# Optimization experiments

Hardware: AMD Instinct MI355X
Metric: run time of the kernel (lower is better)

The kernel has to match this reference:

```python
import jax, jax.numpy as jnp
import numpy as np


def _relative_index(ih: int, iw: int) -> np.ndarray:
    # Static precompute mirroring the torch buffer.
    yy, xx = np.meshgrid(np.arange(ih), np.arange(iw), indexing='ij')
    coords = np.stack([yy.ravel(), xx.ravel()])                 # [2, n]
    rel = coords[:, :, None] - coords[:, None, :]               # [2, n, n]
    rel[0] += ih - 1
    rel[1] += iw - 1
    rel[0] *= 2 * iw - 1
    return rel.sum(0).ravel()                                   # [n*n]


def setup_inputs() -> dict:
    key = jax.random.key(0)
    ks = jax.random.split(key, 5)
    B, N, INP, OUP, HEADS = 64, 256, 512, 512, 16
    ih = iw = 16
    return {
        'x': jax.random.normal(ks[0], (B, N, INP), jnp.float32),
        'w_qkv': jax.random.normal(ks[1], (INP, 3 * OUP), jnp.float32) * 0.02,
        'rel_bias_table': jax.random.normal(ks[2], ((2 * ih - 1) * (2 * iw - 1), HEADS), jnp.float32) * 0.02,
        'w_out': jax.random.normal(ks[3], (OUP, OUP), jnp.float32) * 0.02,
        'b_out': jax.random.normal(ks[4], (OUP,), jnp.float32) * 0.02,
        'ih': ih,
        'iw': iw,
    }


def reference(x, w_qkv, rel_bias_table, w_out, b_out, ih, iw):
    B, N, _ = x.shape
    heads = rel_bias_table.shape[1]
    oup = w_out.shape[0]
    dim_head = oup // heads
    scale = dim_head ** -0.5

    qkv = jnp.einsum('bni,ij->bnj', x, w_qkv)                   # [B, N, 3*oup]
    q, k, v = jnp.split(qkv, 3, axis=-1)
    split_heads = lambda t: t.reshape(B, N, heads, dim_head).transpose(0, 2, 1, 3)
    q, k, v = split_heads(q), split_heads(k), split_heads(v)    # [B, H, N, D]

    dots = jnp.einsum('bhnd,bhmd->bhnm', q, k) * scale          # [B, H, N, N]
    rel_idx = jnp.asarray(_relative_index(int(ih), int(iw)))    # [N*N]
    bias = rel_bias_table[rel_idx].reshape(N, N, heads)         # gather
    dots = dots + bias.transpose(2, 0, 1)[None]                 # [1, H, N, N]

    attn = jax.nn.softmax(dots, axis=-1)
    out = jnp.einsum('bhnm,bhmd->bhnd', attn, v)                # [B, H, N, D]
    out = out.transpose(0, 2, 1, 3).reshape(B, N, oup)
    return jnp.einsum('bno,op->bnp', out, w_out.T) + b_out
```

## Files before the change

### kernel.cpp

```cpp
#include <hip/hip_runtime.h>
#include <stdint.h>

typedef unsigned short u16;
typedef unsigned int u32;
typedef __attribute__((ext_vector_type(8))) __bf16 bf16x8;
typedef __attribute__((ext_vector_type(2))) u32 u32x2;
typedef __attribute__((ext_vector_type(4))) u32 u32x4;
typedef __attribute__((ext_vector_type(4))) float f32x4;

__device__ __forceinline__ float bf2f(u16 x) { return __uint_as_float(((u32)x) << 16); }
__device__ __forceinline__ u16 f2bf(float f) {
  u32 u = __float_as_uint(f);
  u32 r = (u + 0x7fffu + ((u >> 16) & 1u)) >> 16;
  return (u16)r;
}
__device__ __forceinline__ u16 cvbf(float f) {
  union { __bf16 b; u16 u; } x;
  x.b = (__bf16)f;
  return x.u;
}

__device__ __forceinline__ u32x2 ld8(const u16* p) { return *(const u32x2*)p; }
__device__ __forceinline__ u32x4 ld16(const u16* p) { return *(const u32x4*)p; }
__device__ __forceinline__ bf16x8 mk_frag(u32x2 lo, u32x2 hi) {
  union { bf16x8 v; u32x2 u[2]; } t;
  t.u[0] = lo; t.u[1] = hi;
  return t.v;
}

__device__ __forceinline__ void stage_fm(u16* lds, int ch, u32x4 v) {
  int row = ch >> 2, q = ch & 3;
  *(u32x4*)&lds[(row >> 4) * 512 + q * 128 + (row & 15) * 8] = v;
}

__device__ __forceinline__ bf16x8 frag_fm(const u16* lds, int subtile, int g, int c) {
  union { bf16x8 v; u32x4 u; } t;
  t.u = ld16(&lds[subtile * 512 + g * 128 + c * 8]);
  return t.v;
}

__device__ __forceinline__ void swz_bn_bm(int& bn, int& bm) {
  const u32 nx = gridDim.x, ny = gridDim.y;
  if ((ny & 7u) == 0u) {
    u32 d = blockIdx.y * nx + blockIdx.x;
    u32 xcd = d & 7u, wi = d >> 3;
    bm = (int)(xcd * (ny >> 3) + wi / nx);
    bn = (int)(wi % nx);
  } else {
    bn = blockIdx.x;
    bm = blockIdx.y;
  }
}

__global__ void probe_dtype(const u32* __restrict__ x, u32* __restrict__ flag) {
  if (threadIdx.x == 0 && blockIdx.x == 0) {
    int cnt = 0;
    for (int i = 0; i < 32; ++i) {
      u32 e = (x[i] >> 7) & 0xffu;
      cnt += (e >= 96u && e <= 140u) ? 1 : 0;
    }
    *flag = (cnt == 32) ? 1u : 0u;
  }
}

__global__ __launch_bounds__(256) void conv4(const void* __restrict__ src, u16* __restrict__ dst,
                                             const u32* __restrict__ flag, int n4) {
  const bool isbf = (*flag != 0u);
  const int stride = gridDim.x * 256;
  for (int i = blockIdx.x * 256 + threadIdx.x; i < n4; i += stride) {
    if (isbf) {
      ((u32x2*)dst)[i] = ((const u32x2*)src)[i];
    } else {
      const float* s = (const float*)src + (size_t)i * 4;
      u32x2 o;
      o.x = (u32)f2bf(s[0]) | ((u32)f2bf(s[1]) << 16);
      o.y = (u32)f2bf(s[2]) | ((u32)f2bf(s[3]) << 16);
      ((u32x2*)dst)[i] = o;
    }
  }
}

__global__ __launch_bounds__(256) void bias_prep(const void* __restrict__ table,
                                                 float* __restrict__ biasT,
                                                 const u32* __restrict__ flag) {
  const bool isbf = (*flag != 0u);
  int i = blockIdx.x * 256 + threadIdx.x;
  if (i < 16 * 961) {
    int h = i / 961, idx = i - h * 961;
    float v = isbf ? bf2f(((const u16*)table)[idx * 16 + h])
                   : ((const float*)table)[idx * 16 + h];
    biasT[i] = v * 1.4426950408889634f;
  }
}

__global__ __launch_bounds__(256) void transpose_dt(const void* __restrict__ in,
                                                    u16* __restrict__ out,
                                                    const u32* __restrict__ flag, int R, int C) {
  __shared__ u16 t[32][33];
  const bool isbf = (*flag != 0u);
  int r0 = blockIdx.y * 32, c0 = blockIdx.x * 32;
  int rr = threadIdx.x >> 5, cc = threadIdx.x & 31;
#pragma unroll
  for (int i = 0; i < 4; ++i) {
    size_t idx = (size_t)(r0 + rr + i * 8) * C + c0 + cc;
    t[rr + i * 8][cc] = isbf ? ((const u16*)in)[idx] : f2bf(((const float*)in)[idx]);
  }
  __syncthreads();
#pragma unroll
  for (int i = 0; i < 4; ++i) out[(size_t)(c0 + rr + i * 8) * R + r0 + cc] = t[cc][rr + i * 8];
}

template <bool BIAS>
__global__ __launch_bounds__(256) void gemm_k512(const u16* __restrict__ A,
                                                 const u16* __restrict__ BT,
                                                 const u16* __restrict__ bias,
                                                 void* __restrict__ O, int ldo, int row0g,
                                                 const u32* __restrict__ flag) {
  constexpr int K = 512;
  constexpr int NT = 16;
  __shared__ u16 As[128 * 32];
  __shared__ u16 Bs[128 * 32];
  const int tid = threadIdx.x;
  const int wave = tid >> 6, lane = tid & 63;
  const int c = lane & 15, g = lane >> 4;
  const int wm = wave >> 1, wn = wave & 1;
  int bn, bm;
  swz_bn_bm(bn, bm);

  const u16* Ab = A + (size_t)bm * 128 * K;
  const u16* Bb = BT + (size_t)bn * 128 * K;

  const int row0 = tid >> 2, q0 = tid & 3;
  const u16* Asrc0 = Ab + (size_t)row0 * K + q0 * 8;
  const u16* Bsrc0 = Bb + (size_t)row0 * K + q0 * 8;
  const u16* Asrc1 = Asrc0 + (size_t)64 * K;
  const u16* Bsrc1 = Bsrc0 + (size_t)64 * K;

  f32x4 acc[4][4] = {};

  u32x4 a0 = ld16(Asrc0), b0 = ld16(Bsrc0), a1 = ld16(Asrc1), b1 = ld16(Bsrc1);

#pragma unroll
  for (int t = 0; t < NT; ++t) {
    if (t > 0) {
      asm volatile("s_waitcnt lgkmcnt(0)" ::: "memory");
      __builtin_amdgcn_s_barrier();
      __builtin_amdgcn_sched_barrier(0);
    }
    stage_fm(As, tid, a0);
    stage_fm(Bs, tid, b0);
    stage_fm(As, tid + 256, a1);
    stage_fm(Bs, tid + 256, b1);
    if (t + 1 < NT) {
      const int k0 = (t + 1) * 32;
      a0 = ld16(Asrc0 + k0);
      b0 = ld16(Bsrc0 + k0);
      a1 = ld16(Asrc1 + k0);
      b1 = ld16(Bsrc1 + k0);
    }
    asm volatile("s_waitcnt lgkmcnt(0)" ::: "memory");
    __builtin_amdgcn_s_barrier();
    __builtin_amdgcn_sched_barrier(0);

    bf16x8 af[4], bfr[4];
#pragma unroll
    for (int i = 0; i < 4; ++i) {
      af[i] = frag_fm(As, wm * 4 + i, g, c);
      bfr[i] = frag_fm(Bs, wn * 4 + i, g, c);
    }
#pragma unroll
    for (int i = 0; i < 4; ++i)
#pragma unroll
      for (int j = 0; j < 4; ++j)
        acc[i][j] = __builtin_amdgcn_mfma_f32_16x16x32_bf16(af[i], bfr[j], acc[i][j], 0, 0, 0);
  }

  const bool isbf = BIAS ? (*flag != 0u) : true;
#pragma unroll
  for (int i = 0; i < 4; ++i)
#pragma unroll
    for (int j = 0; j < 4; ++j) {
      int jg = bn * 128 + wn * 64 + j * 16 + c;
      float bv = BIAS ? bf2f(bias[jg]) : 0.0f;
#pragma unroll
      for (int r = 0; r < 4; ++r) {
        int mg = bm * 128 + wm * 64 + i * 16 + 4 * g + r;
        float v = acc[i][j][r] + bv;
        size_t off = (size_t)(row0g + mg) * ldo + jg;
        if (BIAS) {
          if (isbf) ((u16*)O)[off] = f2bf(v);
          else ((float*)O)[off] = v;
        } else {
          ((u16*)O)[off] = f2bf(v);
        }
      }
    }
}

__global__ __launch_bounds__(256) void attn_kernel(const u16* __restrict__ qkv,
                                                   const float* __restrict__ biasT,
                                                   u16* __restrict__ Out) {
  __shared__ u16 smem[18432];
  float* biasS = (float*)&smem[16384];

  const int tid = threadIdx.x;
  const int wave = tid >> 6, lane = tid & 63;
  const int c = lane & 15, g = lane >> 4;
  const int half = blockIdx.x & 1;
  const int h = (blockIdx.x >> 1) & 15;
  const int b = blockIdx.x >> 5;

  const u16* xb = qkv + (size_t)b * 256 * 1536;

  u32x4 kvr[4];
#pragma unroll
  for (int i = 0; i < 4; ++i) {
    int ch = tid + i * 256;
    int m = ch >> 2;
    kvr[i] = ld16(xb + (size_t)m * 1536 + 512 + h * 32 + (ch & 3) * 8);
  }
#pragma unroll
  for (int i = 0; i < 4; ++i) stage_fm(smem, tid + i * 256, kvr[i]);

#pragma unroll
  for (int i = 0; i < 16; ++i) {
    int e2 = tid + i * 256;
    int n = e2 >> 4, d = (e2 & 15) * 2;
    u32 val = *(const u32*)(xb + (size_t)n * 1536 + 1024 + h * 32 + d);
    smem[8192 + d * 256 + (n ^ (8 * (d & 7)))] = (u16)(val & 0xffffu);
    smem[8192 + (d + 1) * 256 + (n ^ (8 * ((d + 1) & 7)))] = (u16)(val >> 16);
  }
  for (int i = tid; i < 961; i += 256) biasS[i] = biasT[h * 961 + i];

  u32x4 qv[2];
#pragma unroll
  for (int rg = 0; rg < 2; ++rg) {
    const u16* qp = xb + (size_t)((half * 2 + rg) * 64 + wave * 16 + c) * 1536 + h * 32 + 8 * g;
    qv[rg] = ld16(qp);
  }
  __syncthreads();

  const u16* Vt = &smem[8192];
  const int va = 8 * (c & 7);
  const float scale2 = 0.25503484f;
  const float* bp0 = biasS + wave * 31 + c + 12 - 4 * g;

#pragma unroll
  for (int rg = 0; rg < 2; ++rg) {
    const int rgg = half * 2 + rg;
    union { bf16x8 v; u32x4 u; } qt;
    qt.u = qv[rg];
    bf16x8 qf = qt.v;

    f32x4 o0 = {0.f, 0.f, 0.f, 0.f}, o1 = {0.f, 0.f, 0.f, 0.f};
    float smm = 0.f;

#pragma unroll
    for (int ph = 0; ph < 2; ++ph) {
      f32x4 s[8];
#pragma unroll
      for (int f = 0; f < 8; ++f) {
        bf16x8 kf = frag_fm(smem, ph * 8 + f, g, c);
        f32x4 z = {0.f, 0.f, 0.f, 0.f};
        s[f] = __builtin_amdgcn_mfma_f32_16x16x32_bf16(kf, qf, z, 0, 0, 0);
      }

      float u[8];
#pragma unroll
      for (int f = 0; f < 8; ++f) {
        const int fg = ph * 8 + f;
#pragma unroll
        for (int j = 0; j < 4; ++j) {
          float bv = bp0[(rgg * 4 - fg + 15) * 31 + 3 - j];
          s[f][j] = __builtin_amdgcn_exp2f(s[f][j] * scale2 + bv);
        }
        u[f] = (s[f][0] + s[f][1]) + (s[f][2] + s[f][3]);
      }
      smm += ((u[0] + u[4]) + (u[1] + u[5])) + ((u[2] + u[6]) + (u[3] + u[7]));

#pragma unroll
      for (int q = 0; q < 4; ++q) {
        bf16x8 pf;
        pf[0] = (__bf16)s[2 * q][0]; pf[1] = (__bf16)s[2 * q][1];
        pf[2] = (__bf16)s[2 * q][2]; pf[3] = (__bf16)s[2 * q][3];
        pf[4] = (__bf16)s[2 * q + 1][0]; pf[5] = (__bf16)s[2 * q + 1][1];
        pf[6] = (__bf16)s[2 * q + 1][2]; pf[7] = (__bf16)s[2 * q + 1][3];
        const int kg = (ph * 4 + q) * 32;
        bf16x8 v0 = mk_frag(ld8(&Vt[c * 256 + ((kg + 4 * g) ^ va)]),
                            ld8(&Vt[c * 256 + ((kg + 16 + 4 * g) ^ va)]));
        bf16x8 v1 = mk_frag(ld8(&Vt[(16 + c) * 256 + ((kg + 4 * g) ^ va)]),
                            ld8(&Vt[(16 + c) * 256 + ((kg + 16 + 4 * g) ^ va)]));
        o0 = __builtin_amdgcn_mfma_f32_16x16x32_bf16(pf, v0, o0, 0, 0, 0);
        o1 = __builtin_amdgcn_mfma_f32_16x16x32_bf16(pf, v1, o1, 0, 0, 0);
      }
    }

    smm += __shfl_xor(smm, 16, 64);
    smm += __shfl_xor(smm, 32, 64);
    const float invc = __builtin_amdgcn_rcpf(smm);

    const int nb = rgg * 64 + wave * 16 + 4 * g;
#pragma unroll
    for (int j = 0; j < 4; ++j) {
      int n = nb + j;
      size_t off = ((size_t)b * 256 + n) * 512 + h * 32;
      Out[off + c] = cvbf(o0[j] * invc);
      Out[off + 16 + c] = cvbf(o1[j] * invc);
    }
  }
}

extern "C" void kernel_launch(void* const* d_in, const int* in_sizes, int n_in, void* d_out,
                              int out_size, void* d_ws, size_t ws_size, hipStream_t stream) {
  (void)in_sizes; (void)n_in; (void)out_size;
  const void* x = d_in[0];
  const void* w_qkv = d_in[1];
  const void* table = d_in[2];
  const void* w_out = d_in[3];
  const void* b_out = d_in[4];

  char* ws = (char*)d_ws;
  u32* flag = (u32*)ws;
  u16* xc = (u16*)(ws + 256);
  u16* wqkvT = (u16*)(ws + 16777472);
  float* biasT = (float*)(ws + 18350336);
  u16* woC = (u16*)(ws + 18411840);
  u16* bC = (u16*)(ws + 18936128);
  const size_t DYN = 18937344;
  int CB = 64;
  while (CB > 1 && DYN + (size_t)CB * 1048576 > ws_size) CB >>= 1;
  u16* qkv = (u16*)(ws + DYN);
  u16* att = (u16*)(ws + DYN + (size_t)CB * 786432);

  dim3 blk(256);
  probe_dtype<<<dim3(1), dim3(64), 0, stream>>>((const u32*)x, flag);
  conv4<<<dim3(2048), blk, 0, stream>>>(x, xc, flag, 2097152);
  conv4<<<dim3(256), blk, 0, stream>>>(w_out, woC, flag, 65536);
  conv4<<<dim3(1), blk, 0, stream>>>(b_out, bC, flag, 128);
  bias_prep<<<dim3(61), blk, 0, stream>>>(table, biasT, flag);
  transpose_dt<<<dim3(48, 16), blk, 0, stream>>>(w_qkv, wqkvT, flag, 512, 1536);

  for (int s0 = 0; s0 < 64; s0 += CB) {
    const u16* xcc = xc + (size_t)s0 * 256 * 512;
    gemm_k512<false><<<dim3(12, CB * 2), blk, 0, stream>>>(xcc, wqkvT, nullptr, qkv, 1536, 0,
                                                           flag);
    attn_kernel<<<dim3(CB * 32), blk, 0, stream>>>(qkv, biasT, att);
    gemm_k512<true><<<dim3(4, CB * 2), blk, 0, stream>>>(att, woC, bC, d_out, 512, s0 * 256,
                                                         flag);
  }
}
```

Before: 130.1 us.

## Read K directly from global memory to shrink LDS and raise occupancy

Drops K staging into shared memory. Each wave now loads its K fragments straight from global memory (L2/L1) inside the QK loop, which cuts LDS from about 36KB to 20KB and sets launch bounds to 8 blocks per CU. The Q prefetch moves into the row-group loop, the rg loop is no longer unrolled, and the row-sum is split into two accumulators, all to reduce register pressure. The cost is that K is loaded from global once per row group instead of once per block, so K fragments are read twice with higher latency on the critical path.

```diff
diff --git a/kernel.cpp b/kernel.cpp
--- a/kernel.cpp
+++ b/kernel.cpp
@@ -197,11 +197,11 @@
     }
 }
 
-__global__ __launch_bounds__(256) void attn_kernel(const u16* __restrict__ qkv,
-                                                   const float* __restrict__ biasT,
-                                                   u16* __restrict__ Out) {
-  __shared__ u16 smem[18432];
-  float* biasS = (float*)&smem[16384];
+__global__ __launch_bounds__(256, 8) void attn_kernel(const u16* __restrict__ qkv,
+                                                      const float* __restrict__ biasT,
+                                                      u16* __restrict__ Out) {
+  __shared__ u16 smem[10240];
+  float* biasS = (float*)&smem[8192];
 
   const int tid = threadIdx.x;
   const int wave = tid >> 6, lane = tid & 63;
@@ -212,60 +212,45 @@
 
   const u16* xb = qkv + (size_t)b * 256 * 1536;
 
-  u32x4 kvr[4];
-#pragma unroll
-  for (int i = 0; i < 4; ++i) {
-    int ch = tid + i * 256;
-    int m = ch >> 2;
-    kvr[i] = ld16(xb + (size_t)m * 1536 + 512 + h * 32 + (ch & 3) * 8);
-  }
-#pragma unroll
-  for (int i = 0; i < 4; ++i) stage_fm(smem, tid + i * 256, kvr[i]);
-
 #pragma unroll
   for (int i = 0; i < 16; ++i) {
     int e2 = tid + i * 256;
     int n = e2 >> 4, d = (e2 & 15) * 2;
     u32 val = *(const u32*)(xb + (size_t)n * 1536 + 1024 + h * 32 + d);
-    smem[8192 + d * 256 + (n ^ (8 * (d & 7)))] = (u16)(val & 0xffffu);
-    smem[8192 + (d + 1) * 256 + (n ^ (8 * ((d + 1) & 7)))] = (u16)(val >> 16);
+    smem[d * 256 + (n ^ (8 * (d & 7)))] = (u16)(val & 0xffffu);
+    smem[(d + 1) * 256 + (n ^ (8 * ((d + 1) & 7)))] = (u16)(val >> 16);
   }
   for (int i = tid; i < 961; i += 256) biasS[i] = biasT[h * 961 + i];
-
-  u32x4 qv[2];
-#pragma unroll
-  for (int rg = 0; rg < 2; ++rg) {
-    const u16* qp = xb + (size_t)((half * 2 + rg) * 64 + wave * 16 + c) * 1536 + h * 32 + 8 * g;
-    qv[rg] = ld16(qp);
-  }
   __syncthreads();
 
-  const u16* Vt = &smem[8192];
+  const u16* Vt = &smem[0];
   const int va = 8 * (c & 7);
   const float scale2 = 0.25503484f;
   const float* bp0 = biasS + wave * 31 + c + 12 - 4 * g;
-
-#pragma unroll
+  const u16* kcol = xb + (size_t)c * 1536 + 512 + h * 32 + 8 * g;
+
   for (int rg = 0; rg < 2; ++rg) {
     const int rgg = half * 2 + rg;
     union { bf16x8 v; u32x4 u; } qt;
-    qt.u = qv[rg];
+    qt.u = ld16(xb + (size_t)(rgg * 64 + wave * 16 + c) * 1536 + h * 32 + 8 * g);
     bf16x8 qf = qt.v;
 
     f32x4 o0 = {0.f, 0.f, 0.f, 0.f}, o1 = {0.f, 0.f, 0.f, 0.f};
-    float smm = 0.f;
+    float smA = 0.f, smB = 0.f;
 
 #pragma unroll
     for (int ph = 0; ph < 2; ++ph) {
       f32x4 s[8];
+      const u16* kp = kcol + (size_t)(ph * 8) * 24576;
 #pragma unroll
       for (int f = 0; f < 8; ++f) {
-        bf16x8 kf = frag_fm(smem, ph * 8 + f, g, c);
+        union { bf16x8 v; u32x4 u; } kt;
+        kt.u = ld16(kp);
+        kp += 24576;
         f32x4 z = {0.f, 0.f, 0.f, 0.f};
-        s[f] = __builtin_amdgcn_mfma_f32_16x16x32_bf16(kf, qf, z, 0, 0, 0);
+        s[f] = __builtin_amdgcn_mfma_f32_16x16x32_bf16(kt.v, qf, z, 0, 0, 0);
       }
 
-      float u[8];
 #pragma unroll
       for (int f = 0; f < 8; ++f) {
         const int fg = ph * 8 + f;
@@ -274,9 +259,9 @@
           float bv = bp0[(rgg * 4 - fg + 15) * 31 + 3 - j];
           s[f][j] = __builtin_amdgcn_exp2f(s[f][j] * scale2 + bv);
         }
-        u[f] = (s[f][0] + s[f][1]) + (s[f][2] + s[f][3]);
+        if (f & 1) smB += (s[f][0] + s[f][1]) + (s[f][2] + s[f][3]);
+        else smA += (s[f][0] + s[f][1]) + (s[f][2] + s[f][3]);
       }
-      smm += ((u[0] + u[4]) + (u[1] + u[5])) + ((u[2] + u[6]) + (u[3] + u[7]));
 
 #pragma unroll
       for (int q = 0; q < 4; ++q) {
@@ -295,6 +280,7 @@
       }
     }
 
+    float smm = smA + smB;
     smm += __shfl_xor(smm, 16, 64);
     smm += __shfl_xor(smm, 32, 64);
     const float invc = __builtin_amdgcn_rcpf(smm);
```

New measurement: 333.5 us. +156.4%, slower.
